# Optimization experiments

Hardware: AMD Instinct MI355X
Metric: run time of the kernel (lower is better)

## Reference

```python
import jax, jax.numpy as jnp
import numpy as np

N, E, D, H, HID = 50000, 400000, 64, 8, 1024
NEG_SLOPE = 0.2
BN_EPS = 1e-5


def setup_inputs() -> dict:
    key = jax.random.key(0)
    ks = jax.random.split(key, 10)
    s = 0.05
    return {
        "x": jax.random.normal(ks[0], (N, D), jnp.float32),
        "src": jax.random.randint(ks[1], (E,), 0, N, jnp.int32),
        "dst": jax.random.randint(ks[2], (E,), 0, N, jnp.int32),
        "fc_w": jax.random.normal(ks[3], (H * D, D), jnp.float32) * s,
        "attn_l": jax.random.normal(ks[4], (H, D), jnp.float32) * s,
        "attn_r": jax.random.normal(ks[5], (H, D), jnp.float32) * s,
        "gat_bias": jnp.zeros((H * D,), jnp.float32),
        "bn1_gamma": jnp.ones((H * D,), jnp.float32),
        "bn1_beta": jnp.zeros((H * D,), jnp.float32),
        "w1": jax.random.normal(ks[6], (HID, H * D), jnp.float32) * s,
        "b1": jnp.zeros((HID,), jnp.float32),
        "w2": jax.random.normal(ks[7], (D, HID), jnp.float32) * s,
        "b2": jnp.zeros((D,), jnp.float32),
        "bn2_gamma": jnp.ones((D,), jnp.float32),
        "bn2_beta": jnp.zeros((D,), jnp.float32),
    }


def _batchnorm(h, gamma, beta):
    # training-mode BatchNorm1d: batch statistics over node axis
    mu = h.mean(axis=0)
    var = h.var(axis=0)
    return gamma * (h - mu) * jax.lax.rsqrt(var + BN_EPS) + beta


def reference(x, src, dst, fc_w, attn_l, attn_r, gat_bias,
              bn1_gamma, bn1_beta, w1, b1, w2, b2, bn2_gamma, bn2_beta):
    n = x.shape[0]
    nh, dh = attn_l.shape
    # --- GATConv ---
    feat = (x @ fc_w.T).reshape(n, nh, dh)                 # [N,H,Dh]
    el = jnp.einsum("nhd,hd->nh", feat, attn_l)            # [N,H]
    er = jnp.einsum("nhd,hd->nh", feat, attn_r)            # [N,H]
    e = jax.nn.leaky_relu(el[src] + er[dst], NEG_SLOPE)    # [E,H]
    # edge softmax grouped by destination node (numerically stable)
    emax = jax.ops.segment_max(e, dst, num_segments=n)
    emax = jnp.where(jnp.isfinite(emax), emax, 0.0)        # nodes w/ no in-edges
    ez = jnp.exp(e - emax[dst])
    denom = jax.ops.segment_sum(ez, dst, num_segments=n)
    alpha = ez / denom[dst]                                # [E,H]
    msg = alpha[:, :, None] * feat[src]                    # [E,H,Dh]
    rst = jax.ops.segment_sum(msg, dst, num_segments=n)    # [N,H,Dh]
    rst = rst + gat_bias.reshape(nh, dh)
    h = rst.reshape(n, nh * dh)                            # flatten(1)
    # --- feed forward: BN -> Linear -> ReLU -> Linear -> BN ---
    h = _batchnorm(h, bn1_gamma, bn1_beta)
    h = jax.nn.relu(h @ w1.T + b1)
    h = h @ w2.T + b2
    h = _batchnorm(h, bn2_gamma, bn2_beta)
    return h
```

## Files before the change

### kernel.cpp

```cpp
#include <hip/hip_runtime.h>

#define NEG_SLOPE 0.2f
#define BN_EPS 1e-5f

typedef __bf16 bf16x8 __attribute__((ext_vector_type(8)));
typedef float  f32x4  __attribute__((ext_vector_type(4)));
typedef unsigned short ushort8_t __attribute__((ext_vector_type(8)));

__device__ __forceinline__ unsigned short f2bf(float f) {
    unsigned int u = __float_as_uint(f);
    unsigned int r = u + 0x7FFFu + ((u >> 16) & 1u);
    return (unsigned short)(r >> 16);
}
__device__ __forceinline__ float bf2f(unsigned short u) {
    return __uint_as_float(((unsigned int)u) << 16);
}
__device__ __forceinline__ void gload16(const void* g, void* l) {
    __builtin_amdgcn_global_load_lds(
        (const __attribute__((address_space(1))) unsigned int*)g,
        (__attribute__((address_space(3))) unsigned int*)l, 16, 0, 0);
}

__global__ __launch_bounds__(256)
void prep(const float* __restrict__ x, const int* __restrict__ dst,
          const float* __restrict__ fc_w, const float* __restrict__ w2,
          const float* __restrict__ attn_l, const float* __restrict__ attn_r,
          unsigned short* __restrict__ xbf, unsigned short* __restrict__ fcwbf,
          unsigned short* __restrict__ w2bf, float* __restrict__ proj,
          int* __restrict__ counts, int totX4, int E,
          int bCvtx, int bHist, int bFcw, int bW2)
{
    const int bid = blockIdx.x, tid = threadIdx.x;
    if (bid < bCvtx) {
        int i4 = bid * 256 + tid;
        if (i4 < totX4) {
            float4 v = *(const float4*)(x + (size_t)i4 * 4);
            ushort4 o = {f2bf(v.x), f2bf(v.y), f2bf(v.z), f2bf(v.w)};
            *(ushort4*)(xbf + (size_t)i4 * 4) = o;
        }
    } else if (bid < bHist) {
        int base = (bid - bCvtx) * 1024 + tid;
        #pragma unroll
        for (int k = 0; k < 4; ++k) {
            int e = base + k * 256;
            if (e < E) atomicAdd(&counts[dst[e]], 1);
        }
    } else if (bid < bFcw) {
        int i4 = (bid - bHist) * 256 + tid;
        if (i4 < 8192) {
            float4 v = *(const float4*)(fc_w + (size_t)i4 * 4);
            ushort4 o = {f2bf(v.x), f2bf(v.y), f2bf(v.z), f2bf(v.w)};
            *(ushort4*)(fcwbf + (size_t)i4 * 4) = o;
        }
    } else if (bid < bW2) {
        int i4 = (bid - bFcw) * 256 + tid;
        if (i4 < 16384) {
            float4 v = *(const float4*)(w2 + (size_t)i4 * 4);
            ushort4 o = {f2bf(v.x), f2bf(v.y), f2bf(v.z), f2bf(v.w)};
            *(ushort4*)(w2bf + (size_t)i4 * 4) = o;
        }
    } else {
        for (int t2 = tid; t2 < 512; t2 += 256) {
            int h = t2 >> 6, k = t2 & 63;
            float al = 0.f, ar = 0.f;
            for (int d = 0; d < 64; ++d) {
                float w = fc_w[(size_t)(h * 64 + d) * 64 + k];
                al = fmaf(attn_l[h * 64 + d], w, al);
                ar = fmaf(attn_r[h * 64 + d], w, ar);
            }
            proj[t2] = al;
            proj[512 + t2] = ar;
        }
    }
}

__global__ __launch_bounds__(256)
void scan_elr(const int* __restrict__ counts, int* __restrict__ bsum,
              int* __restrict__ row_ptr, int* __restrict__ cursor, int N, int NB,
              const unsigned short* __restrict__ xbf, const float* __restrict__ proj,
              float* __restrict__ el, float* __restrict__ er, int NH)
{
    if ((int)blockIdx.x < NB) {
        __shared__ int sm[256];
        __shared__ int rm[256];
        int i = blockIdx.x * 256 + threadIdx.x;
        int v = (i < N) ? counts[i] : 0;
        sm[threadIdx.x] = v;
        __syncthreads();
        #pragma unroll
        for (int d = 1; d < 256; d <<= 1) {
            int t = (threadIdx.x >= d) ? sm[threadIdx.x - d] : 0;
            __syncthreads();
            sm[threadIdx.x] += t;
            __syncthreads();
        }
        if (threadIdx.x == 255)
            atomicExch(&bsum[blockIdx.x], sm[255] | 0x40000000);
        int myagg = 0;
        if ((int)threadIdx.x < (int)blockIdx.x) {
            int vv;
            do { vv = atomicAdd(&bsum[threadIdx.x], 0); } while (!(vv & 0x40000000));
            myagg = vv & 0x3FFFFFFF;
        }
        rm[threadIdx.x] = myagg;
        __syncthreads();
        #pragma unroll
        for (int d = 128; d > 0; d >>= 1) {
            if (threadIdx.x < d) rm[threadIdx.x] += rm[threadIdx.x + d];
            __syncthreads();
        }
        int pre = rm[0];
        if (i < N) {
            int w = sm[threadIdx.x] + pre;
            row_ptr[i + 1] = w;
            cursor[i + 1] = w;
        }
        if (i == 0) { row_ptr[0] = 0; cursor[0] = 0; }
    } else {
        int idx = (blockIdx.x - NB) * 256 + threadIdx.x;
        if (idx >= NH) return;
        int h = idx & 7, n = idx >> 3;
        const ushort8_t* f = (const ushort8_t*)(xbf + (size_t)n * 64);
        const float* pl = proj + h * 64;
        const float* pr = proj + 512 + h * 64;
        float sl = 0.f, sr = 0.f;
        #pragma unroll
        for (int i8 = 0; i8 < 8; ++i8) {
            ushort8_t v = f[i8];
            #pragma unroll
            for (int t = 0; t < 8; ++t) {
                float fv = bf2f(v[t]);
                sl = fmaf(fv, pl[i8 * 8 + t], sl);
                sr = fmaf(fv, pr[i8 * 8 + t], sr);
            }
        }
        el[idx] = sl;
        er[idx] = sr;
    }
}

__global__ void scatter_edges(const int* __restrict__ src, const int* __restrict__ dst,
                              int* __restrict__ cursor, int* __restrict__ esrc, int E) {
    int e = blockIdx.x * 256 + threadIdx.x;
    if (e < E) {
        int p = atomicAdd(&cursor[dst[e]], 1);
        esrc[p] = src[e];
    }
}

__global__ __launch_bounds__(256)
void gat_aggregate(const int* __restrict__ row_ptr, const int* __restrict__ esrc,
                   const float* __restrict__ el, const float* __restrict__ er,
                   const unsigned short* __restrict__ xb, unsigned short* __restrict__ xagg,
                   int N)
{
    int node = blockIdx.x * 4 + (threadIdx.x >> 6);
    if (node >= N) return;
    const int lane = threadIdx.x & 63;
    const int h = lane >> 3, j = lane & 7;
    const int beg = row_ptr[node], end = row_ptr[node + 1];
    const float er_n = er[node * 8 + h];

    float denom = 0.f;
    float a[8] = {};
    int s_cur = (beg < end) ? esrc[beg] : 0;
    for (int k = beg; k < end; ++k) {
        int s_nxt = (k + 1 < end) ? esrc[k + 1] : 0;
        float elv = el[s_cur * 8 + h];
        ushort8_t fv = *(const ushort8_t*)(xb + (size_t)s_cur * 64 + j * 8);
        float v = elv + er_n;
        v = (v > 0.f) ? v : NEG_SLOPE * v;
        float z = __expf(v);
        denom += z;
        #pragma unroll
        for (int t = 0; t < 8; ++t) a[t] = fmaf(z, bf2f(fv[t]), a[t]);
        s_cur = s_nxt;
    }
    float inv = (end > beg) ? 1.f / denom : 0.f;
    ushort8_t o;
    #pragma unroll
    for (int t = 0; t < 8; ++t) o[t] = f2bf(a[t] * inv);
    *(ushort8_t*)(xagg + (size_t)node * 512 + lane * 8) = o;
}

__global__ __launch_bounds__(256)
void bn1_stats(const unsigned short* __restrict__ Xa,
               const unsigned short* __restrict__ Fw,
               const float* __restrict__ gat_bias,
               float* __restrict__ sums1, int M)
{
    __shared__ alignas(16) char Asm[128 * 64 * 2];
    __shared__ alignas(16) char Bsm[64 * 64 * 2];
    __shared__ float reds[4][64], redq[4][64];
    const int tid = threadIdx.x, lane = tid & 63, wave = tid >> 6;
    const int bm = blockIdx.x * 128;
    const int head = blockIdx.y;
    const int lr = lane >> 3, lk = ((lane & 7) ^ lr) * 8;

    #pragma unroll
    for (int it = 0; it < 4; ++it) {
        int seg = wave * 4 + it;
        gload16(Xa + (size_t)(bm + seg * 8 + lr) * 512 + head * 64 + lk, Asm + seg * 1024);
    }
    #pragma unroll
    for (int it = 0; it < 2; ++it) {
        int seg = wave * 2 + it;
        gload16(Fw + (size_t)(head * 64 + seg * 8 + lr) * 64 + lk, Bsm + seg * 1024);
    }
    __syncthreads();

    f32x4 acc[2][4] = {};
    #pragma unroll
    for (int kk = 0; kk < 2; ++kk) {
        int kg = kk * 4 + (lane >> 4);
        bf16x8 a[2], b[4];
        #pragma unroll
        for (int i = 0; i < 2; ++i) {
            int row = wave * 32 + i * 16 + (lane & 15);
            a[i] = *(const bf16x8*)(Asm + row * 128 + ((kg ^ (row & 7)) << 4));
        }
        #pragma unroll
        for (int j = 0; j < 4; ++j) {
            int row = j * 16 + (lane & 15);
            b[j] = *(const bf16x8*)(Bsm + row * 128 + ((kg ^ (row & 7)) << 4));
        }
        #pragma unroll
        for (int i = 0; i < 2; ++i)
            #pragma unroll
            for (int j = 0; j < 4; ++j)
                acc[i][j] = __builtin_amdgcn_mfma_f32_16x16x32_bf16(a[i], b[j], acc[i][j], 0, 0, 0);
    }

    float s4[4] = {}, q4[4] = {};
    #pragma unroll
    for (int j = 0; j < 4; ++j) {
        int col = j * 16 + (lane & 15);
        float bias = gat_bias[head * 64 + col];
        #pragma unroll
        for (int i = 0; i < 2; ++i)
            #pragma unroll
            for (int r = 0; r < 4; ++r) {
                int gm = bm + wave * 32 + i * 16 + (lane >> 4) * 4 + r;
                if (gm < M) {
                    float vq = bf2f(f2bf(acc[i][j][r] + bias));
                    s4[j] += vq; q4[j] += vq * vq;
                }
            }
    }
    #pragma unroll
    for (int j = 0; j < 4; ++j) {
        s4[j] += __shfl_xor(s4[j], 16); q4[j] += __shfl_xor(q4[j], 16);
        s4[j] += __shfl_xor(s4[j], 32); q4[j] += __shfl_xor(q4[j], 32);
    }
    if (lane < 16) {
        #pragma unroll
        for (int j = 0; j < 4; ++j) {
            reds[wave][j * 16 + lane] = s4[j];
            redq[wave][j * 16 + lane] = q4[j];
        }
    }
    __syncthreads();
    if (wave == 0 && lane < 16) {
        #pragma unroll
        for (int j = 0; j < 4; ++j) {
            int c = j * 16 + lane;
            atomicAdd(&sums1[head * 64 + c], reds[0][c] + reds[1][c] + reds[2][c] + reds[3][c]);
            atomicAdd(&sums1[512 + head * 64 + c], redq[0][c] + redq[1][c] + redq[2][c] + redq[3][c]);
        }
    }
}

__global__ __launch_bounds__(256)
void fold(const float* __restrict__ w1, const float* __restrict__ fc_w,
          const float* __restrict__ sums1, const float* __restrict__ gamma,
          const float* __restrict__ beta, const float* __restrict__ gat_bias,
          const float* __restrict__ b1, unsigned short* __restrict__ wtil,
          float* __restrict__ b1p, float invM)
{
    const int bid = blockIdx.x, tid = threadIdx.x;
    if (bid < 64) {
        __shared__ float sF[64][65];
        __shared__ float sa[64];
        int ot = bid >> 3, h = bid & 7;
        if (tid < 64) {
            int c = h * 64 + tid;
            float mu = sums1[c] * invM;
            float var = sums1[512 + c] * invM - mu * mu;
            sa[tid] = gamma[c] * rsqrtf(var + BN_EPS);
        }
        for (int e = 0; e < 16; ++e) {
            int idx = tid * 16 + e;
            int d = idx >> 6, k = idx & 63;
            sF[k][d] = fc_w[(size_t)(h * 64 + d) * 64 + k];
        }
        __syncthreads();
        int ol = tid >> 1, half = tid & 1;
        int o = ot * 128 + ol;
        int kbase = half * 32;
        float acc[32];
        #pragma unroll
        for (int i = 0; i < 32; ++i) acc[i] = 0.f;
        const float* wrow = w1 + (size_t)o * 512 + h * 64;
        #pragma unroll
        for (int dc = 0; dc < 4; ++dc) {
            float wa[16];
            #pragma unroll
            for (int d = 0; d < 16; ++d) wa[d] = wrow[dc * 16 + d] * sa[dc * 16 + d];
            #pragma unroll
            for (int kk2 = 0; kk2 < 32; ++kk2) {
                float s = acc[kk2];
                #pragma unroll
                for (int d = 0; d < 16; ++d) s = fmaf(wa[d], sF[kbase + kk2][dc * 16 + d], s);
                acc[kk2] = s;
            }
        }
        unsigned int* orow = (unsigned int*)(wtil + (size_t)o * 512 + h * 64 + kbase);
        #pragma unroll
        for (int i = 0; i < 16; ++i)
            orow[i] = (unsigned int)f2bf(acc[2 * i]) | ((unsigned int)f2bf(acc[2 * i + 1]) << 16);
    } else {
        __shared__ float ss[512];
        for (int c = tid; c < 512; c += 256) {
            float mu = sums1[c] * invM;
            float var = sums1[512 + c] * invM - mu * mu;
            float a = gamma[c] * rsqrtf(var + BN_EPS);
            ss[c] = beta[c] + a * (gat_bias[c] - mu);
        }
        __syncthreads();
        int wave = tid >> 6, lane = tid & 63;
        int o = (bid - 64) * 4 + wave;
        const float* wrow = w1 + (size_t)o * 512 + lane * 8;
        float p = 0.f;
        #pragma unroll
        for (int t2 = 0; t2 < 8; ++t2) p = fmaf(wrow[t2], ss[lane * 8 + t2], p);
        #pragma unroll
        for (int d = 1; d < 64; d <<= 1) p += __shfl_xor(p, d);
        if (lane == 0) b1p[o] = b1[o] + p;
    }
}

__global__ __launch_bounds__(256)
void gemm2p(const unsigned short* __restrict__ A,
            const unsigned short* __restrict__ B,
            const unsigned short* __restrict__ W2,
            const float* __restrict__ b1p,
            unsigned short* __restrict__ P,
            int M)
{
    __shared__ alignas(16) char smem[49152];
    char* Abuf0 = smem;
    char* Abuf1 = smem + 16384;
    char* Bbuf  = smem + 32768;
    char* TR   = smem;
    char* Wbuf = smem + 32768;
    char* PK   = smem + 32768;

    const int tid = threadIdx.x, lane = tid & 63, wave = tid >> 6;
    const int wr = wave >> 1, wc = wave & 1;
    const int lr = lane >> 3, lk = ((lane & 7) ^ lr) * 8;

    int bid = blockIdx.x;
    int wgid = (bid & 7) * 391 + (bid >> 3);
    const int bm = (wgid >> 3) * 128;
    const int t  = wgid & 7;
    const int bn = t * 128;

    #pragma unroll
    for (int it = 0; it < 4; ++it) {
        int seg = wave * 4 + it;
        gload16(A + (size_t)(bm + seg * 8 + lr) * 512 + lk, Abuf0 + seg * 1024);
    }

    f32x4 acc[4][4] = {};
    #pragma unroll
    for (int ks = 0; ks < 8; ++ks) {
        const int k0 = ks * 64;
        #pragma unroll
        for (int it = 0; it < 4; ++it) {
            int seg = wave * 4 + it;
            gload16(B + (size_t)(bn + seg * 8 + lr) * 512 + k0 + lk, Bbuf + seg * 1024);
        }
        if (ks < 7) {
            char* An = (ks & 1) ? Abuf0 : Abuf1;
            #pragma unroll
            for (int it = 0; it < 4; ++it) {
                int seg = wave * 4 + it;
                gload16(A + (size_t)(bm + seg * 8 + lr) * 512 + (k0 + 64) + lk, An + seg * 1024);
            }
            asm volatile("s_waitcnt vmcnt(4)" ::: "memory");
        } else {
            asm volatile("s_waitcnt vmcnt(0)" ::: "memory");
        }
        __builtin_amdgcn_s_barrier();
        __builtin_amdgcn_sched_barrier(0);
        const char* Ac = (ks & 1) ? Abuf1 : Abuf0;
        #pragma unroll
        for (int kk = 0; kk < 2; ++kk) {
            int kg = kk * 4 + (lane >> 4);
            bf16x8 a[4], b[4];
            #pragma unroll
            for (int i = 0; i < 4; ++i) {
                int row = wr * 64 + i * 16 + (lane & 15);
                a[i] = *(const bf16x8*)(Ac + row * 128 + ((kg ^ (row & 7)) << 4));
            }
            #pragma unroll
            for (int j = 0; j < 4; ++j) {
                int row = wc * 64 + j * 16 + (lane & 15);
                b[j] = *(const bf16x8*)(Bbuf + row * 128 + ((kg ^ (row & 7)) << 4));
            }
            #pragma unroll
            for (int i = 0; i < 4; ++i)
                #pragma unroll
                for (int j = 0; j < 4; ++j)
                    acc[i][j] = __builtin_amdgcn_mfma_f32_16x16x32_bf16(a[i], b[j], acc[i][j], 0, 0, 0);
        }
        __builtin_amdgcn_sched_barrier(0);
        __builtin_amdgcn_s_barrier();
        __builtin_amdgcn_sched_barrier(0);
    }

    #pragma unroll
    for (int j = 0; j < 4; ++j) {
        int c = wc * 64 + j * 16 + (lane & 15);
        float bs = b1p[bn + c];
        #pragma unroll
        for (int i = 0; i < 4; ++i)
            #pragma unroll
            for (int r = 0; r < 4; ++r) {
                int rw = wr * 64 + i * 16 + (lane >> 4) * 4 + r;
                float v = fmaxf(acc[i][j][r] + bs, 0.f);
                *(unsigned short*)(TR + rw * 256 + (((c >> 3) ^ (rw & 7)) << 4) + (c & 7) * 2) = f2bf(v);
            }
    }
    #pragma unroll
    for (int it = 0; it < 4; ++it) {
        int oc = wave * 16 + it * 4 + (lane >> 4);
        int g = lane & 15;
        gload16(W2 + (size_t)oc * 1024 + bn + ((g ^ (oc & 7))) * 8, Wbuf + (wave * 4 + it) * 1024);
    }
    __syncthreads();

    f32x4 pacc[2][4] = {};
    #pragma unroll
    for (int ks = 0; ks < 4; ++ks) {
        int kg2 = ks * 4 + (lane >> 4);
        #pragma unroll
        for (int i = 0; i < 2; ++i) {
            int arow = wave * 32 + i * 16 + (lane & 15);
            bf16x8 av = *(const bf16x8*)(TR + arow * 256 + ((kg2 ^ (arow & 7)) << 4));
            #pragma unroll
            for (int j = 0; j < 4; ++j) {
                int oc = j * 16 + (lane & 15);
                bf16x8 bv = *(const bf16x8*)(Wbuf + oc * 256 + ((kg2 ^ (oc & 7)) << 4));
                pacc[i][j] = __builtin_amdgcn_mfma_f32_16x16x32_bf16(av, bv, pacc[i][j], 0, 0, 0);
            }
        }
    }
    __syncthreads();

    #pragma unroll
    for (int i = 0; i < 2; ++i)
        #pragma unroll
        for (int j = 0; j < 4; ++j)
            #pragma unroll
            for (int r = 0; r < 4; ++r) {
                int row = wave * 32 + i * 16 + (lane >> 4) * 4 + r;
                int col = j * 16 + (lane & 15);
                *(unsigned short*)(PK + row * 128 + col * 2) = f2bf(pacc[i][j][r]);
            }
    __syncthreads();
    unsigned short* Pt = P + (size_t)t * M * 64;
    #pragma unroll
    for (int it = 0; it < 4; ++it) {
        int u = it * 256 + tid;
        int row = u >> 3, g8 = u & 7;
        int gm = bm + row;
        if (gm < M) {
            uint4 v = *(const uint4*)(PK + row * 128 + g8 * 16);
            *(uint4*)(Pt + (size_t)gm * 64 + g8 * 8) = v;
        }
    }
}

__global__ __launch_bounds__(256)
void reduce_bn2(const unsigned short* __restrict__ P, const float* __restrict__ b2,
                float* __restrict__ out, int M, float* __restrict__ sums2)
{
    __shared__ float ls[256], lq[256];
    int c = threadIdx.x & 63, g = threadIdx.x >> 6;
    const size_t S = (size_t)M * 64;
    float bias = b2[c];
    float s = 0.f, q = 0.f;
    for (int r = blockIdx.x * 4 + g; r < M; r += gridDim.x * 4) {
        size_t idx = (size_t)r * 64 + c;
        float v = bias;
        #pragma unroll
        for (int t = 0; t < 8; ++t) v += bf2f(P[t * S + idx]);
        out[idx] = v;
        s += v; q += v * v;
    }
    ls[threadIdx.x] = s; lq[threadIdx.x] = q;
    __syncthreads();
    if (g == 0) {
        s = ls[c] + ls[64 + c] + ls[128 + c] + ls[192 + c];
        q = lq[c] + lq[64 + c] + lq[128 + c] + lq[192 + c];
        atomicAdd(&sums2[c], s);
        atomicAdd(&sums2[64 + c], q);
    }
}

__global__ __launch_bounds__(256)
void bn_apply64(float* __restrict__ X, const float* __restrict__ sums2,
                const float* __restrict__ gamma, const float* __restrict__ beta,
                int M, float invM)
{
    int c = threadIdx.x & 63, g = threadIdx.x >> 6;
    float mu = sums2[c] * invM;
    float var = sums2[64 + c] * invM - mu * mu;
    float a = gamma[c] * rsqrtf(var + BN_EPS);
    float b = beta[c] - a * mu;
    for (int r = blockIdx.x * 4 + g; r < M; r += gridDim.x * 4) {
        size_t i = (size_t)r * 64 + c;
        X[i] = fmaf(a, X[i], b);
    }
}

extern "C" void kernel_launch(void* const* d_in, const int* in_sizes, int n_in,
                              void* d_out, int out_size, void* d_ws, size_t ws_size,
                              hipStream_t stream)
{
    const float* x         = (const float*)d_in[0];
    const int*   src       = (const int*)d_in[1];
    const int*   dst       = (const int*)d_in[2];
    const float* fc_w      = (const float*)d_in[3];
    const float* attn_l    = (const float*)d_in[4];
    const float* attn_r    = (const float*)d_in[5];
    const float* gat_bias  = (const float*)d_in[6];
    const float* bn1_gamma = (const float*)d_in[7];
    const float* bn1_beta  = (const float*)d_in[8];
    const float* w1        = (const float*)d_in[9];
    const float* b1        = (const float*)d_in[10];
    const float* w2        = (const float*)d_in[11];
    const float* b2        = (const float*)d_in[12];
    const float* bn2_gamma = (const float*)d_in[13];
    const float* bn2_beta  = (const float*)d_in[14];
    float* out = (float*)d_out;

    const int D = 64, HD = 512, HID = 1024;
    const int N = in_sizes[0] / D;
    const int E = in_sizes[1];
    const int NH = N * 8;
    const int NB = (N + 255) / 256;
    const int Mpad = ((N + 127) / 128) * 128 + 128;

    size_t off = 0;
    auto alloc = [&](size_t bytes) -> void* {
        void* p = (char*)d_ws + off;
        off += (bytes + 255) & ~(size_t)255;
        return p;
    };
    unsigned short* xagg = (unsigned short*)alloc((size_t)Mpad * HD * 2);
    unsigned short* P    = (unsigned short*)alloc((size_t)8 * N * D * 2);
    unsigned short* xbf  = (unsigned short*)alloc((size_t)N * D * 2);
    unsigned short* fcwbf = (unsigned short*)alloc((size_t)HD * D * 2);
    unsigned short* wtil = (unsigned short*)alloc((size_t)HID * HD * 2);
    unsigned short* w2bf = (unsigned short*)alloc((size_t)D * HID * 2);
    float* b1p   = (float*)alloc(HID * 4);
    float* proj  = (float*)alloc(2 * 512 * 4);
    float* el    = (float*)alloc((size_t)NH * 4);
    float* er    = (float*)alloc((size_t)NH * 4);
    char* zbase  = (char*)d_ws + off;
    int* counts  = (int*)alloc((size_t)N * 4);
    float* sums1 = (float*)alloc(2 * 512 * 4);
    float* sums2 = (float*)alloc(2 * 64 * 4);
    int* bsum    = (int*)alloc(256 * 4);
    size_t zbytes = ((char*)d_ws + off) - zbase;
    int* row_ptr = (int*)alloc((size_t)(N + 1) * 4);
    int* cursor  = (int*)alloc((size_t)(N + 1) * 4);
    int* esrc    = (int*)alloc((size_t)E * 4);
    (void)ws_size; (void)n_in; (void)out_size;

    hipMemsetAsync(zbase, 0, zbytes, stream);

    {
        int totX4 = (N * D) / 4;
        int bCvtx = (totX4 + 255) / 256;
        int bHist = bCvtx + (E + 1023) / 1024;
        int bFcw  = bHist + 32;
        int bW2   = bFcw + 64;
        int grid  = bW2 + 1;
        prep<<<grid, 256, 0, stream>>>(x, dst, fc_w, w2, attn_l, attn_r,
                                       xbf, fcwbf, w2bf, proj, counts,
                                       totX4, E, bCvtx, bHist, bFcw, bW2);
    }

    scan_elr<<<NB + (NH + 255) / 256, 256, 0, stream>>>(counts, bsum, row_ptr, cursor,
                                                        N, NB, xbf, proj, el, er, NH);
    scatter_edges<<<(E + 255) / 256, 256, 0, stream>>>(src, dst, cursor, esrc, E);

    gat_aggregate<<<(N + 3) / 4, 256, 0, stream>>>(row_ptr, esrc, el, er, xbf, xagg, N);

    {
        dim3 grid((N + 127) / 128, 8);
        bn1_stats<<<grid, 256, 0, stream>>>(xagg, fcwbf, gat_bias, sums1, N);
    }
    fold<<<320, 256, 0, stream>>>(w1, fc_w, sums1, bn1_gamma, bn1_beta, gat_bias,
                                  b1, wtil, b1p, 1.f / N);

    {
        int nwg = ((N + 127) / 128) * 8;
        gemm2p<<<nwg, 256, 0, stream>>>(xagg, wtil, w2bf, b1p, P, N);
    }

    reduce_bn2<<<1024, 256, 0, stream>>>(P, b2, out, N, sums2);
    bn_apply64<<<1024, 256, 0, stream>>>(out, sums2, bn2_gamma, bn2_beta, N, 1.f / N);
}
```

Measured before the change: 291.1 us.

## Fuse pipeline stages into persistent kernels with software grid barriers

```diff
diff --git a/kernel.cpp b/kernel.cpp
--- a/kernel.cpp
+++ b/kernel.cpp
@@ -20,322 +20,347 @@
         (const __attribute__((address_space(1))) unsigned int*)g,
         (__attribute__((address_space(3))) unsigned int*)l, 16, 0, 0);
 }
-
-__global__ __launch_bounds__(256)
-void prep(const float* __restrict__ x, const int* __restrict__ dst,
-          const float* __restrict__ fc_w, const float* __restrict__ w2,
-          const float* __restrict__ attn_l, const float* __restrict__ attn_r,
-          unsigned short* __restrict__ xbf, unsigned short* __restrict__ fcwbf,
-          unsigned short* __restrict__ w2bf, float* __restrict__ proj,
-          int* __restrict__ counts, int totX4, int E,
-          int bCvtx, int bHist, int bFcw, int bW2)
+__device__ __forceinline__ void gsync(int* cnt, int target) {
+    __syncthreads();
+    if (threadIdx.x == 0) {
+        __threadfence();
+        atomicAdd(cnt, 1);
+        while (atomicAdd(cnt, 0) < target) { asm volatile("s_sleep 1"); }
+        __threadfence();
+    }
+    __syncthreads();
+}
+
+__global__ __launch_bounds__(256, 4)
+void front(const float* __restrict__ x, const int* __restrict__ src,
+           const int* __restrict__ dst,
+           const float* __restrict__ fc_w, const float* __restrict__ w2,
+           const float* __restrict__ attn_l, const float* __restrict__ attn_r,
+           unsigned short* __restrict__ xbf, unsigned short* __restrict__ fcwbf,
+           unsigned short* __restrict__ w2bf, float* __restrict__ proj,
+           int* __restrict__ counts, int* __restrict__ bsum,
+           int* __restrict__ row_ptr, int* __restrict__ cursor,
+           int* __restrict__ esrc, float* __restrict__ el, float* __restrict__ er,
+           unsigned short* __restrict__ xagg, int* __restrict__ cnt,
+           int N, int E, int NB)
 {
     const int bid = blockIdx.x, tid = threadIdx.x;
-    if (bid < bCvtx) {
-        int i4 = bid * 256 + tid;
-        if (i4 < totX4) {
-            float4 v = *(const float4*)(x + (size_t)i4 * 4);
-            ushort4 o = {f2bf(v.x), f2bf(v.y), f2bf(v.z), f2bf(v.w)};
-            *(ushort4*)(xbf + (size_t)i4 * 4) = o;
-        }
-    } else if (bid < bHist) {
-        int base = (bid - bCvtx) * 1024 + tid;
-        #pragma unroll
-        for (int k = 0; k < 4; ++k) {
-            int e = base + k * 256;
-            if (e < E) atomicAdd(&counts[dst[e]], 1);
-        }
-    } else if (bid < bFcw) {
-        int i4 = (bid - bHist) * 256 + tid;
-        if (i4 < 8192) {
-            float4 v = *(const float4*)(fc_w + (size_t)i4 * 4);
-            ushort4 o = {f2bf(v.x), f2bf(v.y), f2bf(v.z), f2bf(v.w)};
-            *(ushort4*)(fcwbf + (size_t)i4 * 4) = o;
-        }
-    } else if (bid < bW2) {
-        int i4 = (bid - bFcw) * 256 + tid;
-        if (i4 < 16384) {
-            float4 v = *(const float4*)(w2 + (size_t)i4 * 4);
-            ushort4 o = {f2bf(v.x), f2bf(v.y), f2bf(v.z), f2bf(v.w)};
-            *(ushort4*)(w2bf + (size_t)i4 * 4) = o;
-        }
-    } else {
-        for (int t2 = tid; t2 < 512; t2 += 256) {
-            int h = t2 >> 6, k = t2 & 63;
-            float al = 0.f, ar = 0.f;
-            for (int d = 0; d < 64; ++d) {
-                float w = fc_w[(size_t)(h * 64 + d) * 64 + k];
-                al = fmaf(attn_l[h * 64 + d], w, al);
-                ar = fmaf(attn_r[h * 64 + d], w, ar);
-            }
-            proj[t2] = al;
-            proj[512 + t2] = ar;
-        }
-    }
-}
-
-__global__ __launch_bounds__(256)
-void scan_elr(const int* __restrict__ counts, int* __restrict__ bsum,
-              int* __restrict__ row_ptr, int* __restrict__ cursor, int N, int NB,
-              const unsigned short* __restrict__ xbf, const float* __restrict__ proj,
-              float* __restrict__ el, float* __restrict__ er, int NH)
-{
-    if ((int)blockIdx.x < NB) {
+    const int grid = gridDim.x;
+    const int NH = N * 8;
+    const int totX4 = (N * 64) / 4;
+    const int bCvtx = (totX4 + 255) / 256;
+    const int bHist = bCvtx + (E + 1023) / 1024;
+    const int bFcw  = bHist + 32;
+    const int bW2   = bFcw + 64;
+    const int nPrep = bW2 + 1;
+
+    for (int c = bid; c < nPrep; c += grid) {
+        if (c < bCvtx) {
+            int i4 = c * 256 + tid;
+            if (i4 < totX4) {
+                float4 v = *(const float4*)(x + (size_t)i4 * 4);
+                ushort4 o = {f2bf(v.x), f2bf(v.y), f2bf(v.z), f2bf(v.w)};
+                *(ushort4*)(xbf + (size_t)i4 * 4) = o;
+            }
+        } else if (c < bHist) {
+            int base = (c - bCvtx) * 1024 + tid;
+            #pragma unroll
+            for (int k = 0; k < 4; ++k) {
+                int e = base + k * 256;
+                if (e < E) atomicAdd(&counts[dst[e]], 1);
+            }
+        } else if (c < bFcw) {
+            int i4 = (c - bHist) * 256 + tid;
+            if (i4 < 8192) {
+                float4 v = *(const float4*)(fc_w + (size_t)i4 * 4);
+                ushort4 o = {f2bf(v.x), f2bf(v.y), f2bf(v.z), f2bf(v.w)};
+                *(ushort4*)(fcwbf + (size_t)i4 * 4) = o;
+            }
+        } else if (c < bW2) {
+            int i4 = (c - bFcw) * 256 + tid;
+            if (i4 < 16384) {
+                float4 v = *(const float4*)(w2 + (size_t)i4 * 4);
+                ushort4 o = {f2bf(v.x), f2bf(v.y), f2bf(v.z), f2bf(v.w)};
+                *(ushort4*)(w2bf + (size_t)i4 * 4) = o;
+            }
+        } else {
+            for (int t2 = tid; t2 < 512; t2 += 256) {
+                int h = t2 >> 6, k = t2 & 63;
+                float al = 0.f, ar = 0.f;
+                for (int d = 0; d < 64; ++d) {
+                    float w = fc_w[(size_t)(h * 64 + d) * 64 + k];
+                    al = fmaf(attn_l[h * 64 + d], w, al);
+                    ar = fmaf(attn_r[h * 64 + d], w, ar);
+                }
+                proj[t2] = al;
+                proj[512 + t2] = ar;
+            }
+        }
+    }
+    gsync(cnt, grid);
+
+    if (bid < NB) {
         __shared__ int sm[256];
         __shared__ int rm[256];
-        int i = blockIdx.x * 256 + threadIdx.x;
+        int i = bid * 256 + tid;
         int v = (i < N) ? counts[i] : 0;
-        sm[threadIdx.x] = v;
+        sm[tid] = v;
         __syncthreads();
         #pragma unroll
         for (int d = 1; d < 256; d <<= 1) {
-            int t = (threadIdx.x >= d) ? sm[threadIdx.x - d] : 0;
-            __syncthreads();
-            sm[threadIdx.x] += t;
-            __syncthreads();
-        }
-        if (threadIdx.x == 255)
-            atomicExch(&bsum[blockIdx.x], sm[255] | 0x40000000);
+            int t = (tid >= d) ? sm[tid - d] : 0;
+            __syncthreads();
+            sm[tid] += t;
+            __syncthreads();
+        }
+        if (tid == 255) atomicExch(&bsum[bid], sm[255] | 0x40000000);
         int myagg = 0;
-        if ((int)threadIdx.x < (int)blockIdx.x) {
+        if (tid < bid) {
             int vv;
-            do { vv = atomicAdd(&bsum[threadIdx.x], 0); } while (!(vv & 0x40000000));
+            do { vv = atomicAdd(&bsum[tid], 0); } while (!(vv & 0x40000000));
             myagg = vv & 0x3FFFFFFF;
         }
-        rm[threadIdx.x] = myagg;
+        rm[tid] = myagg;
         __syncthreads();
         #pragma unroll
         for (int d = 128; d > 0; d >>= 1) {
-            if (threadIdx.x < d) rm[threadIdx.x] += rm[threadIdx.x + d];
+            if (tid < d) rm[tid] += rm[tid + d];
             __syncthreads();
         }
         int pre = rm[0];
         if (i < N) {
-            int w = sm[threadIdx.x] + pre;
+            int w = sm[tid] + pre;
             row_ptr[i + 1] = w;
             cursor[i + 1] = w;
         }
         if (i == 0) { row_ptr[0] = 0; cursor[0] = 0; }
     } else {
-        int idx = (blockIdx.x - NB) * 256 + threadIdx.x;
-        if (idx >= NH) return;
-        int h = idx & 7, n = idx >> 3;
-        const ushort8_t* f = (const ushort8_t*)(xbf + (size_t)n * 64);
-        const float* pl = proj + h * 64;
-        const float* pr = proj + 512 + h * 64;
-        float sl = 0.f, sr = 0.f;
-        #pragma unroll
-        for (int i8 = 0; i8 < 8; ++i8) {
-            ushort8_t v = f[i8];
-            #pragma unroll
-            for (int t = 0; t < 8; ++t) {
-                float fv = bf2f(v[t]);
-                sl = fmaf(fv, pl[i8 * 8 + t], sl);
-                sr = fmaf(fv, pr[i8 * 8 + t], sr);
-            }
-        }
-        el[idx] = sl;
-        er[idx] = sr;
-    }
-}
-
-__global__ void scatter_edges(const int* __restrict__ src, const int* __restrict__ dst,
-                              int* __restrict__ cursor, int* __restrict__ esrc, int E) {
-    int e = blockIdx.x * 256 + threadIdx.x;
-    if (e < E) {
-        int p = atomicAdd(&cursor[dst[e]], 1);
-        esrc[p] = src[e];
-    }
-}
-
-__global__ __launch_bounds__(256)
-void gat_aggregate(const int* __restrict__ row_ptr, const int* __restrict__ esrc,
-                   const float* __restrict__ el, const float* __restrict__ er,
-                   const unsigned short* __restrict__ xb, unsigned short* __restrict__ xagg,
-                   int N)
+        const int EC = (NH + 255) / 256;
+        for (int c = bid - NB; c < EC; c += grid - NB) {
+            int idx = c * 256 + tid;
+            if (idx >= NH) continue;
+            int h = idx & 7, n = idx >> 3;
+            const ushort8_t* f = (const ushort8_t*)(xbf + (size_t)n * 64);
+            const float* pl = proj + h * 64;
+            const float* pr = proj + 512 + h * 64;
+            float sl = 0.f, sr = 0.f;
+            #pragma unroll
+            for (int i8 = 0; i8 < 8; ++i8) {
+                ushort8_t v = f[i8];
+                #pragma unroll
+                for (int t = 0; t < 8; ++t) {
+                    float fv = bf2f(v[t]);
+                    sl = fmaf(fv, pl[i8 * 8 + t], sl);
+                    sr = fmaf(fv, pr[i8 * 8 + t], sr);
+                }
+            }
+            el[idx] = sl;
+            er[idx] = sr;
+        }
+    }
+    gsync(cnt, 2 * grid);
+
+    {
+        const int SC = (E + 255) / 256;
+        for (int c = bid; c < SC; c += grid) {
+            int e = c * 256 + tid;
+            if (e < E) {
+                int p = atomicAdd(&cursor[dst[e]], 1);
+                esrc[p] = src[e];
+            }
+        }
+    }
+    gsync(cnt, 3 * grid);
+
+    {
+        const int NG = (N + 3) / 4;
+        const int lane = tid & 63;
+        const int h = lane >> 3, j = lane & 7;
+        for (int g = bid; g < NG; g += grid) {
+            int node = g * 4 + (tid >> 6);
+            if (node >= N) continue;
+            const int beg = row_ptr[node], end = row_ptr[node + 1];
+            const float er_n = er[node * 8 + h];
+            float denom = 0.f;
+            float a[8] = {};
+            int s_cur = (beg < end) ? esrc[beg] : 0;
+            for (int k = beg; k < end; ++k) {
+                int s_nxt = (k + 1 < end) ? esrc[k + 1] : 0;
+                float elv = el[s_cur * 8 + h];
+                ushort8_t fv = *(const ushort8_t*)(xbf + (size_t)s_cur * 64 + j * 8);
+                float v = elv + er_n;
+                v = (v > 0.f) ? v : NEG_SLOPE * v;
+                float z = __expf(v);
+                denom += z;
+                #pragma unroll
+                for (int t = 0; t < 8; ++t) a[t] = fmaf(z, bf2f(fv[t]), a[t]);
+                s_cur = s_nxt;
+            }
+            float inv = (end > beg) ? 1.f / denom : 0.f;
+            ushort8_t o;
+            #pragma unroll
+            for (int t = 0; t < 8; ++t) o[t] = f2bf(a[t] * inv);
+            *(ushort8_t*)(xagg + (size_t)node * 512 + lane * 8) = o;
+        }
+    }
+}
+
+__global__ __launch_bounds__(256, 4)
+void mid(const unsigned short* __restrict__ Xa, const unsigned short* __restrict__ Fw,
+         const float* __restrict__ gat_bias,
+         const float* __restrict__ w1, const float* __restrict__ fc_w,
+         const float* __restrict__ gamma, const float* __restrict__ beta,
+         const float* __restrict__ b1,
+         float* __restrict__ sums1, unsigned short* __restrict__ wtil,
+         float* __restrict__ b1p, int* __restrict__ cnt, int M, float invM)
 {
-    int node = blockIdx.x * 4 + (threadIdx.x >> 6);
-    if (node >= N) return;
-    const int lane = threadIdx.x & 63;
-    const int h = lane >> 3, j = lane & 7;
-    const int beg = row_ptr[node], end = row_ptr[node + 1];
-    const float er_n = er[node * 8 + h];
-
-    float denom = 0.f;
-    float a[8] = {};
-    int s_cur = (beg < end) ? esrc[beg] : 0;
-    for (int k = beg; k < end; ++k) {
-        int s_nxt = (k + 1 < end) ? esrc[k + 1] : 0;
-        float elv = el[s_cur * 8 + h];
-        ushort8_t fv = *(const ushort8_t*)(xb + (size_t)s_cur * 64 + j * 8);
-        float v = elv + er_n;
-        v = (v > 0.f) ? v : NEG_SLOPE * v;
-        float z = __expf(v);
-        denom += z;
-        #pragma unroll
-        for (int t = 0; t < 8; ++t) a[t] = fmaf(z, bf2f(fv[t]), a[t]);
-        s_cur = s_nxt;
-    }
-    float inv = (end > beg) ? 1.f / denom : 0.f;
-    ushort8_t o;
-    #pragma unroll
-    for (int t = 0; t < 8; ++t) o[t] = f2bf(a[t] * inv);
-    *(ushort8_t*)(xagg + (size_t)node * 512 + lane * 8) = o;
-}
-
-__global__ __launch_bounds__(256)
-void bn1_stats(const unsigned short* __restrict__ Xa,
-               const unsigned short* __restrict__ Fw,
-               const float* __restrict__ gat_bias,
-               float* __restrict__ sums1, int M)
-{
-    __shared__ alignas(16) char Asm[128 * 64 * 2];
-    __shared__ alignas(16) char Bsm[64 * 64 * 2];
+    __shared__ alignas(16) char msm[26624];
     __shared__ float reds[4][64], redq[4][64];
-    const int tid = threadIdx.x, lane = tid & 63, wave = tid >> 6;
-    const int bm = blockIdx.x * 128;
-    const int head = blockIdx.y;
-    const int lr = lane >> 3, lk = ((lane & 7) ^ lr) * 8;
-
-    #pragma unroll
-    for (int it = 0; it < 4; ++it) {
-        int seg = wave * 4 + it;
-        gload16(Xa + (size_t)(bm + seg * 8 + lr) * 512 + head * 64 + lk, Asm + seg * 1024);
-    }
-    #pragma unroll
-    for (int it = 0; it < 2; ++it) {
-        int seg = wave * 2 + it;
-        gload16(Fw + (size_t)(head * 64 + seg * 8 + lr) * 64 + lk, Bsm + seg * 1024);
-    }
-    __syncthreads();
-
-    f32x4 acc[2][4] = {};
-    #pragma unroll
-    for (int kk = 0; kk < 2; ++kk) {
-        int kg = kk * 4 + (lane >> 4);
-        bf16x8 a[2], b[4];
-        #pragma unroll
-        for (int i = 0; i < 2; ++i) {
-            int row = wave * 32 + i * 16 + (lane & 15);
-            a[i] = *(const bf16x8*)(Asm + row * 128 + ((kg ^ (row & 7)) << 4));
-        }
-        #pragma unroll
-        for (int j = 0; j < 4; ++j) {
-            int row = j * 16 + (lane & 15);
-            b[j] = *(const bf16x8*)(Bsm + row * 128 + ((kg ^ (row & 7)) << 4));
-        }
-        #pragma unroll
-        for (int i = 0; i < 2; ++i)
-            #pragma unroll
-            for (int j = 0; j < 4; ++j)
-                acc[i][j] = __builtin_amdgcn_mfma_f32_16x16x32_bf16(a[i], b[j], acc[i][j], 0, 0, 0);
-    }
-
-    float s4[4] = {}, q4[4] = {};
-    #pragma unroll
-    for (int j = 0; j < 4; ++j) {
-        int col = j * 16 + (lane & 15);
-        float bias = gat_bias[head * 64 + col];
-        #pragma unroll
-        for (int i = 0; i < 2; ++i)
-            #pragma unroll
-            for (int r = 0; r < 4; ++r) {
-                int gm = bm + wave * 32 + i * 16 + (lane >> 4) * 4 + r;
-                if (gm < M) {
-                    float vq = bf2f(f2bf(acc[i][j][r] + bias));
-                    s4[j] += vq; q4[j] += vq * vq;
+    const int bid = blockIdx.x, tid = threadIdx.x;
+    const int grid = gridDim.x;
+    const int lane = tid & 63, wave = tid >> 6;
+
+    {
+        char* Asm = msm;
+        char* Bsm = msm + 16384;
+        const int lr = lane >> 3, lk = ((lane & 7) ^ lr) * 8;
+        const int nJobs = ((M + 127) / 128) * 8;
+        for (int job = bid; job < nJobs; job += grid) {
+            const int bm = (job >> 3) * 128;
+            const int head = job & 7;
+            __syncthreads();
+            #pragma unroll
+            for (int it = 0; it < 4; ++it) {
+                int seg = wave * 4 + it;
+                gload16(Xa + (size_t)(bm + seg * 8 + lr) * 512 + head * 64 + lk, Asm + seg * 1024);
+            }
+            #pragma unroll
+            for (int it = 0; it < 2; ++it) {
+                int seg = wave * 2 + it;
+                gload16(Fw + (size_t)(head * 64 + seg * 8 + lr) * 64 + lk, Bsm + seg * 1024);
+            }
+            __syncthreads();
+            f32x4 acc[2][4] = {};
+            #pragma unroll
+            for (int kk = 0; kk < 2; ++kk) {
+                int kg = kk * 4 + (lane >> 4);
+                bf16x8 a[2], b[4];
+                #pragma unroll
+                for (int i = 0; i < 2; ++i) {
+                    int row = wave * 32 + i * 16 + (lane & 15);
+                    a[i] = *(const bf16x8*)(Asm + row * 128 + ((kg ^ (row & 7)) << 4));
                 }
-            }
-    }
-    #pragma unroll
-    for (int j = 0; j < 4; ++j) {
-        s4[j] += __shfl_xor(s4[j], 16); q4[j] += __shfl_xor(q4[j], 16);
-        s4[j] += __shfl_xor(s4[j], 32); q4[j] += __shfl_xor(q4[j], 32);
-    }
-    if (lane < 16) {
-        #pragma unroll
-        for (int j = 0; j < 4; ++j) {
-            reds[wave][j * 16 + lane] = s4[j];
-            redq[wave][j * 16 + lane] = q4[j];
-        }
-    }
-    __syncthreads();
-    if (wave == 0 && lane < 16) {
-        #pragma unroll
-        for (int j = 0; j < 4; ++j) {
-            int c = j * 16 + lane;
-            atomicAdd(&sums1[head * 64 + c], reds[0][c] + reds[1][c] + reds[2][c] + reds[3][c]);
-            atomicAdd(&sums1[512 + head * 64 + c], redq[0][c] + redq[1][c] + redq[2][c] + redq[3][c]);
-        }
-    }
-}
-
-__global__ __launch_bounds__(256)
-void fold(const float* __restrict__ w1, const float* __restrict__ fc_w,
-          const float* __restrict__ sums1, const float* __restrict__ gamma,
-          const float* __restrict__ beta, const float* __restrict__ gat_bias,
-          const float* __restrict__ b1, unsigned short* __restrict__ wtil,
-          float* __restrict__ b1p, float invM)
-{
-    const int bid = blockIdx.x, tid = threadIdx.x;
-    if (bid < 64) {
-        __shared__ float sF[64][65];
-        __shared__ float sa[64];
-        int ot = bid >> 3, h = bid & 7;
-        if (tid < 64) {
-            int c = h * 64 + tid;
-            float mu = sums1[c] * invM;
-            float var = sums1[512 + c] * invM - mu * mu;
-            sa[tid] = gamma[c] * rsqrtf(var + BN_EPS);
-        }
-        for (int e = 0; e < 16; ++e) {
-            int idx = tid * 16 + e;
-            int d = idx >> 6, k = idx & 63;
-            sF[k][d] = fc_w[(size_t)(h * 64 + d) * 64 + k];
-        }
-        __syncthreads();
-        int ol = tid >> 1, half = tid & 1;
-        int o = ot * 128 + ol;
-        int kbase = half * 32;
-        float acc[32];
-        #pragma unroll
-        for (int i = 0; i < 32; ++i) acc[i] = 0.f;
-        const float* wrow = w1 + (size_t)o * 512 + h * 64;
-        #pragma unroll
-        for (int dc = 0; dc < 4; ++dc) {
-            float wa[16];
-            #pragma unroll
-            for (int d = 0; d < 16; ++d) wa[d] = wrow[dc * 16 + d] * sa[dc * 16 + d];
-            #pragma unroll
-            for (int kk2 = 0; kk2 < 32; ++kk2) {
-                float s = acc[kk2];
-                #pragma unroll
-                for (int d = 0; d < 16; ++d) s = fmaf(wa[d], sF[kbase + kk2][dc * 16 + d], s);
-                acc[kk2] = s;
-            }
-        }
-        unsigned int* orow = (unsigned int*)(wtil + (size_t)o * 512 + h * 64 + kbase);
-        #pragma unroll
-        for (int i = 0; i < 16; ++i)
-            orow[i] = (unsigned int)f2bf(acc[2 * i]) | ((unsigned int)f2bf(acc[2 * i + 1]) << 16);
-    } else {
-        __shared__ float ss[512];
-        for (int c = tid; c < 512; c += 256) {
-            float mu = sums1[c] * invM;
-            float var = sums1[512 + c] * invM - mu * mu;
-            float a = gamma[c] * rsqrtf(var + BN_EPS);
-            ss[c] = beta[c] + a * (gat_bias[c] - mu);
-        }
-        __syncthreads();
-        int wave = tid >> 6, lane = tid & 63;
-        int o = (bid - 64) * 4 + wave;
-        const float* wrow = w1 + (size_t)o * 512 + lane * 8;
-        float p = 0.f;
-        #pragma unroll
-        for (int t2 = 0; t2 < 8; ++t2) p = fmaf(wrow[t2], ss[lane * 8 + t2], p);
-        #pragma unroll
-        for (int d = 1; d < 64; d <<= 1) p += __shfl_xor(p, d);
-        if (lane == 0) b1p[o] = b1[o] + p;
+                #pragma unroll
+                for (int j = 0; j < 4; ++j) {
+                    int row = j * 16 + (lane & 15);
+                    b[j] = *(const bf16x8*)(Bsm + row * 128 + ((kg ^ (row & 7)) << 4));
+                }
+                #pragma unroll
+                for (int i = 0; i < 2; ++i)
+                    #pragma unroll
+                    for (int j = 0; j < 4; ++j)
+                        acc[i][j] = __builtin_amdgcn_mfma_f32_16x16x32_bf16(a[i], b[j], acc[i][j], 0, 0, 0);
+            }
+            float s4[4] = {}, q4[4] = {};
+            #pragma unroll
+            for (int j = 0; j < 4; ++j) {
+                int col = j * 16 + (lane & 15);
+                float bias = gat_bias[head * 64 + col];
+                #pragma unroll
+                for (int i = 0; i < 2; ++i)
+                    #pragma unroll
+                    for (int r = 0; r < 4; ++r) {
+                        int gm = bm + wave * 32 + i * 16 + (lane >> 4) * 4 + r;
+                        if (gm < M) {
+                            float vq = bf2f(f2bf(acc[i][j][r] + bias));
+                            s4[j] += vq; q4[j] += vq * vq;
+                        }
+                    }
+            }
+            #pragma unroll
+            for (int j = 0; j < 4; ++j) {
+                s4[j] += __shfl_xor(s4[j], 16); q4[j] += __shfl_xor(q4[j], 16);
+                s4[j] += __shfl_xor(s4[j], 32); q4[j] += __shfl_xor(q4[j], 32);
+            }
+            if (lane < 16) {
+                #pragma unroll
+                for (int j = 0; j < 4; ++j) {
+                    reds[wave][j * 16 + lane] = s4[j];
+                    redq[wave][j * 16 + lane] = q4[j];
+                }
+            }
+            __syncthreads();
+            if (wave == 0 && lane < 16) {
+                #pragma unroll
+                for (int j = 0; j < 4; ++j) {
+                    int c = j * 16 + lane;
+                    atomicAdd(&sums1[head * 64 + c], reds[0][c] + reds[1][c] + reds[2][c] + reds[3][c]);
+                    atomicAdd(&sums1[512 + head * 64 + c], redq[0][c] + redq[1][c] + redq[2][c] + redq[3][c]);
+                }
+            }
+        }
+    }
+    gsync(cnt, grid);
+
+    for (int job = bid; job < 320; job += grid) {
+        if (job < 64) {
+            float (*sF)[65] = (float(*)[65])msm;
+            float* sa = (float*)(msm + 16640);
+            int ot = job >> 3, h = job & 7;
+            if (tid < 64) {
+                int c = h * 64 + tid;
+                float mu = sums1[c] * invM;
+                float var = sums1[512 + c] * invM - mu * mu;
+                sa[tid] = gamma[c] * rsqrtf(var + BN_EPS);
+            }
+            for (int e = 0; e < 16; ++e) {
+                int idx = tid * 16 + e;
+                int d = idx >> 6, k = idx & 63;
+                sF[k][d] = fc_w[(size_t)(h * 64 + d) * 64 + k];
+            }
+            __syncthreads();
+            int ol = tid >> 1, half = tid & 1;
+            int o = ot * 128 + ol;
+            int kbase = half * 32;
+            float acc[32];
+            #pragma unroll
+            for (int i = 0; i < 32; ++i) acc[i] = 0.f;
+            const float* wrow = w1 + (size_t)o * 512 + h * 64;
+            #pragma unroll
+            for (int dc = 0; dc < 4; ++dc) {
+                float wa[16];
+                #pragma unroll
+                for (int d = 0; d < 16; ++d) wa[d] = wrow[dc * 16 + d] * sa[dc * 16 + d];
+                #pragma unroll
+                for (int kk2 = 0; kk2 < 32; ++kk2) {
+                    float s = acc[kk2];
+                    #pragma unroll
+                    for (int d = 0; d < 16; ++d) s = fmaf(wa[d], sF[kbase + kk2][dc * 16 + d], s);
+                    acc[kk2] = s;
+                }
+            }
+            unsigned int* orow = (unsigned int*)(wtil + (size_t)o * 512 + h * 64 + kbase);
+            #pragma unroll
+            for (int i = 0; i < 16; ++i)
+                orow[i] = (unsigned int)f2bf(acc[2 * i]) | ((unsigned int)f2bf(acc[2 * i + 1]) << 16);
+        } else {
+            float* ss = (float*)msm;
+            for (int c = tid; c < 512; c += 256) {
+                float mu = sums1[c] * invM;
+                float var = sums1[512 + c] * invM - mu * mu;
+                float a = gamma[c] * rsqrtf(var + BN_EPS);
+                ss[c] = beta[c] + a * (gat_bias[c] - mu);
+            }
+            __syncthreads();
+            int o = (job - 64) * 4 + wave;
+            const float* wrow = w1 + (size_t)o * 512 + lane * 8;
+            float p = 0.f;
+            #pragma unroll
+            for (int t2 = 0; t2 < 8; ++t2) p = fmaf(wrow[t2], ss[lane * 8 + t2], p);
+            #pragma unroll
+            for (int d = 1; d < 64; d <<= 1) p += __shfl_xor(p, d);
+            if (lane == 0) b1p[o] = b1[o] + p;
+        }
     }
 }
 
@@ -344,8 +369,7 @@
             const unsigned short* __restrict__ B,
             const unsigned short* __restrict__ W2,
             const float* __restrict__ b1p,
-            unsigned short* __restrict__ P,
-            int M)
+            unsigned short* __restrict__ P, int M)
 {
     __shared__ alignas(16) char smem[49152];
     char* Abuf0 = smem;
@@ -482,46 +506,46 @@
     }
 }
 
-__global__ __launch_bounds__(256)
-void reduce_bn2(const unsigned short* __restrict__ P, const float* __restrict__ b2,
-                float* __restrict__ out, int M, float* __restrict__ sums2)
+__global__ __launch_bounds__(256, 8)
+void back(const unsigned short* __restrict__ P, const float* __restrict__ b2,
+          float* __restrict__ out, const float* __restrict__ gamma,
+          const float* __restrict__ beta, float* __restrict__ sums2,
+          int* __restrict__ cnt, int M, float invM)
 {
     __shared__ float ls[256], lq[256];
+    const int bid = blockIdx.x, grid = gridDim.x;
     int c = threadIdx.x & 63, g = threadIdx.x >> 6;
     const size_t S = (size_t)M * 64;
-    float bias = b2[c];
-    float s = 0.f, q = 0.f;
-    for (int r = blockIdx.x * 4 + g; r < M; r += gridDim.x * 4) {
-        size_t idx = (size_t)r * 64 + c;
-        float v = bias;
-        #pragma unroll
-        for (int t = 0; t < 8; ++t) v += bf2f(P[t * S + idx]);
-        out[idx] = v;
-        s += v; q += v * v;
-    }
-    ls[threadIdx.x] = s; lq[threadIdx.x] = q;
-    __syncthreads();
-    if (g == 0) {
-        s = ls[c] + ls[64 + c] + ls[128 + c] + ls[192 + c];
-        q = lq[c] + lq[64 + c] + lq[128 + c] + lq[192 + c];
-        atomicAdd(&sums2[c], s);
-        atomicAdd(&sums2[64 + c], q);
-    }
-}
-
-__global__ __launch_bounds__(256)
-void bn_apply64(float* __restrict__ X, const float* __restrict__ sums2,
-                const float* __restrict__ gamma, const float* __restrict__ beta,
-                int M, float invM)
-{
-    int c = threadIdx.x & 63, g = threadIdx.x >> 6;
-    float mu = sums2[c] * invM;
-    float var = sums2[64 + c] * invM - mu * mu;
-    float a = gamma[c] * rsqrtf(var + BN_EPS);
-    float b = beta[c] - a * mu;
-    for (int r = blockIdx.x * 4 + g; r < M; r += gridDim.x * 4) {
-        size_t i = (size_t)r * 64 + c;
-        X[i] = fmaf(a, X[i], b);
+    {
+        float bias = b2[c];
+        float s = 0.f, q = 0.f;
+        for (int r = bid * 4 + g; r < M; r += grid * 4) {
+            size_t idx = (size_t)r * 64 + c;
+            float v = bias;
+            #pragma unroll
+            for (int t = 0; t < 8; ++t) v += bf2f(P[t * S + idx]);
+            out[idx] = v;
+            s += v; q += v * v;
+        }
+        ls[threadIdx.x] = s; lq[threadIdx.x] = q;
+        __syncthreads();
+        if (g == 0) {
+            s = ls[c] + ls[64 + c] + ls[128 + c] + ls[192 + c];
+            q = lq[c] + lq[64 + c] + lq[128 + c] + lq[192 + c];
+            atomicAdd(&sums2[c], s);
+            atomicAdd(&sums2[64 + c], q);
+        }
+    }
+    gsync(cnt, grid);
+    {
+        float mu = sums2[c] * invM;
+        float var = sums2[64 + c] * invM - mu * mu;
+        float a = gamma[c] * rsqrtf(var + BN_EPS);
+        float b = beta[c] - a * mu;
+        for (int r = bid * 4 + g; r < M; r += grid * 4) {
+            size_t i = (size_t)r * 64 + c;
+            out[i] = fmaf(a, out[i], b);
+        }
     }
 }
 
@@ -574,44 +598,33 @@
     float* sums1 = (float*)alloc(2 * 512 * 4);
     float* sums2 = (float*)alloc(2 * 64 * 4);
     int* bsum    = (int*)alloc(256 * 4);
+    int* cnts    = (int*)alloc(3 * 256);
     size_t zbytes = ((char*)d_ws + off) - zbase;
     int* row_ptr = (int*)alloc((size_t)(N + 1) * 4);
     int* cursor  = (int*)alloc((size_t)(N + 1) * 4);
     int* esrc    = (int*)alloc((size_t)E * 4);
     (void)ws_size; (void)n_in; (void)out_size;
 
+    int* cnt_front = cnts;
+    int* cnt_mid   = cnts + 64;
+    int* cnt_back  = cnts + 128;
+
     hipMemsetAsync(zbase, 0, zbytes, stream);
 
-    {
-        int totX4 = (N * D) / 4;
-        int bCvtx = (totX4 + 255) / 256;
-        int bHist = bCvtx + (E + 1023) / 1024;
-        int bFcw  = bHist + 32;
-        int bW2   = bFcw + 64;
-        int grid  = bW2 + 1;
-        prep<<<grid, 256, 0, stream>>>(x, dst, fc_w, w2, attn_l, attn_r,
-                                       xbf, fcwbf, w2bf, proj, counts,
-                                       totX4, E, bCvtx, bHist, bFcw, bW2);
-    }
-
-    scan_elr<<<NB + (NH + 255) / 256, 256, 0, stream>>>(counts, bsum, row_ptr, cursor,
-                                                        N, NB, xbf, proj, el, er, NH);
-    scatter_edges<<<(E + 255) / 256, 256, 0, stream>>>(src, dst, cursor, esrc, E);
-
-    gat_aggregate<<<(N + 3) / 4, 256, 0, stream>>>(row_ptr, esrc, el, er, xbf, xagg, N);
-
-    {
-        dim3 grid((N + 127) / 128, 8);
-        bn1_stats<<<grid, 256, 0, stream>>>(xagg, fcwbf, gat_bias, sums1, N);
-    }
-    fold<<<320, 256, 0, stream>>>(w1, fc_w, sums1, bn1_gamma, bn1_beta, gat_bias,
-                                  b1, wtil, b1p, 1.f / N);
+    front<<<960, 256, 0, stream>>>(x, src, dst, fc_w, w2, attn_l, attn_r,
+                                   xbf, fcwbf, w2bf, proj, counts, bsum,
+                                   row_ptr, cursor, esrc, el, er, xagg,
+                                   cnt_front, N, E, NB);
+
+    mid<<<768, 256, 0, stream>>>(xagg, fcwbf, gat_bias, w1, fc_w,
+                                 bn1_gamma, bn1_beta, b1,
+                                 sums1, wtil, b1p, cnt_mid, N, 1.f / N);
 
     {
         int nwg = ((N + 127) / 128) * 8;
         gemm2p<<<nwg, 256, 0, stream>>>(xagg, wtil, w2bf, b1p, P, N);
     }
 
-    reduce_bn2<<<1024, 256, 0, stream>>>(P, b2, out, N, sums2);
-    bn_apply64<<<1024, 256, 0, stream>>>(out, sums2, bn2_gamma, bn2_beta, N, 1.f / N);
-}
+    back<<<1024, 256, 0, stream>>>(P, b2, out, bn2_gamma, bn2_beta, sums2,
+                                   cnt_back, N, 1.f / N);
+}
```

Result: slower. 785.1 us (+169.7%).
